# Performance work log

Measured on AMD Instinct MI355X. Metric: run time of the kernel, lower is better.

Reference implementation:

```python
import jax, jax.numpy as jnp
import numpy as np

K = 2  # num_experts_per_token


def setup_inputs() -> dict:
    key = jax.random.key(0)
    ks = jax.random.split(key, 5)
    B, T, D, E, H = 2, 2048, 768, 8, 1536
    x = jax.random.normal(ks[0], (B, T, D), dtype=jnp.float32)
    gate_w = jax.random.normal(ks[1], (E, D), dtype=jnp.float32) * (1.0 / np.sqrt(D))
    gate_bank = jax.random.normal(ks[2], (E, D, H), dtype=jnp.float32) * (1.0 / np.sqrt(D))
    up_bank = jax.random.normal(ks[3], (E, D, H), dtype=jnp.float32) * (1.0 / np.sqrt(D))
    down_bank = jax.random.normal(ks[4], (E, H, D), dtype=jnp.float32) * (1.0 / np.sqrt(H))
    return {"x": x, "gate_w": gate_w, "gate_bank": gate_bank,
            "up_bank": up_bank, "down_bank": down_bank}


def reference(x, gate_w, gate_bank, up_bank, down_bank):
    # x: [B,T,D]; gate_w: [E,D]; banks: [E,D,H]/[E,D,H]/[E,H,D]
    # Eval mode: no gate noise (module only adds noise when training).
    logits = jnp.einsum('btd,ed->bte', x, gate_w)                  # [B,T,E]
    probs = jax.nn.softmax(logits, axis=-1)
    selected_probs, selected_idx = jax.lax.top_k(probs, K)          # [B,T,K]
    selected_probs = selected_probs / (
        jnp.sum(selected_probs, axis=-1, keepdims=True) + 1e-8)

    a = jnp.einsum('btd,edh->bteh', x, gate_bank)                   # [B,T,E,H]
    u = jnp.einsum('btd,edh->bteh', x, up_bank)
    h = jax.nn.silu(a) * u
    y_all = jnp.einsum('bteh,ehd->bted', h, down_bank)              # [B,T,E,D]

    # Gather the top-k experts' outputs and combine with normalized weights.
    y_sel = jnp.take_along_axis(y_all, selected_idx[..., None], axis=2)  # [B,T,K,D]
    y = jnp.sum(y_sel * selected_probs[..., None], axis=2)          # [B,T,D]
    return y
```

## Files before the change

### kernel.cpp

```cpp
#include <hip/hip_runtime.h>
#include <hip/hip_bf16.h>

#define NTOK 4096
#define DDIM 768
#define EEXP 8
#define HDIM 1536
#define MBLK 128
#define MAXMB 72
#define CAP  (MAXMB * MBLK)
#define NENT (NTOK * 2)
#define RTHREADS 1024
#define EPT (NENT / RTHREADS)

typedef float f32x4 __attribute__((ext_vector_type(4)));
typedef __bf16 bf16x8 __attribute__((ext_vector_type(8)));
typedef __bf16 bf16x4 __attribute__((ext_vector_type(4)));

static const size_t XB_OFF   = 0;
static const size_t GT_OFF   = 6291456;
static const size_t UT_OFF   = GT_OFF + 18874368;
static const size_t YB_OFF   = GT_OFF;
static const size_t DT_OFF   = UT_OFF + 18874368;
static const size_t HB_OFF   = DT_OFF + 18874368;
static const size_t TKI_OFF  = HB_OFF + 28311552;
static const size_t TKW_OFF  = TKI_OFF + NENT*4;
static const size_t PT_OFF   = TKW_OFF + NENT*4;
static const size_t SL_OFF   = PT_OFF + CAP*4;
static const size_t CTRL_OFF = SL_OFF + NENT*4;
static const size_t WS_NEEDED = CTRL_OFF + 1024;

#define GLOAD16(g, l) __builtin_amdgcn_global_load_lds( \
    (const __attribute__((address_space(1))) void*)(g),  \
    (__attribute__((address_space(3))) void*)(l), 16, 0, 0)



__global__ __launch_bounds__(256) void convert_x_kernel(
    const float* __restrict__ x, __bf16* __restrict__ xb, int n4)
{
    int i = blockIdx.x * 256 + threadIdx.x;
    if (i < n4) {
        f32x4 v = reinterpret_cast<const f32x4*>(x)[i];
        bf16x4 o;
        o[0] = (__bf16)v[0]; o[1] = (__bf16)v[1];
        o[2] = (__bf16)v[2]; o[3] = (__bf16)v[3];
        reinterpret_cast<bf16x4*>(xb)[i] = o;
    }
}

__global__ __launch_bounds__(256) void transpose_bf16_kernel(
    const float* __restrict__ src, __bf16* __restrict__ dst, int R, int C)
{
    __shared__ float tile[32][33];
    const float* s = src + (size_t)blockIdx.z * R * C;
    __bf16* d = dst + (size_t)blockIdx.z * R * C;
    int tx = threadIdx.x & 31, ty = threadIdx.x >> 5;
    int r0 = blockIdx.y * 32, c0 = blockIdx.x * 32;
#pragma unroll
    for (int j = 0; j < 4; j++)
        tile[ty + j*8][tx] = s[(size_t)(r0 + ty + j*8) * C + c0 + tx];
    __syncthreads();
#pragma unroll
    for (int j = 0; j < 4; j++)
        d[(size_t)(c0 + ty + j*8) * R + r0 + tx] = (__bf16)tile[tx][ty + j*8];
}

__global__ __launch_bounds__(256) void gating_kernel(
    const float* __restrict__ x, const float* __restrict__ gw,
    int* __restrict__ topk_idx, float* __restrict__ topk_w)
{
    int lane = threadIdx.x & 63;
    int t = blockIdx.x * 4 + (threadIdx.x >> 6);
    const float* xr = x + (size_t)t * DDIM;
    float acc[EEXP];
#pragma unroll
    for (int e = 0; e < EEXP; e++) acc[e] = 0.0f;
    for (int i = 0; i < DDIM / 64; i++) {
        int d = lane + i * 64;
        float xv = xr[d];
#pragma unroll
        for (int e = 0; e < EEXP; e++) acc[e] += xv * gw[e * DDIM + d];
    }
#pragma unroll
    for (int e = 0; e < EEXP; e++) {
        for (int off = 32; off; off >>= 1) acc[e] += __shfl_xor(acc[e], off);
    }
    if (lane == 0) {
        float m = acc[0];
#pragma unroll
        for (int e = 1; e < EEXP; e++) m = fmaxf(m, acc[e]);
        float p[EEXP], sum = 0.0f;
#pragma unroll
        for (int e = 0; e < EEXP; e++) { p[e] = expf(acc[e] - m); sum += p[e]; }
        int i0 = 0; float b0 = acc[0];
#pragma unroll
        for (int e = 1; e < EEXP; e++) if (acc[e] > b0) { b0 = acc[e]; i0 = e; }
        int i1 = -1; float b1 = -3.4e38f;
#pragma unroll
        for (int e = 0; e < EEXP; e++) if (e != i0 && acc[e] > b1) { b1 = acc[e]; i1 = e; }
        float pr0 = p[i0] / sum, pr1 = p[i1] / sum;
        float den = pr0 + pr1 + 1e-8f;
        topk_idx[2*t]   = i0; topk_w[2*t]   = pr0 / den;
        topk_idx[2*t+1] = i1; topk_w[2*t+1] = pr1 / den;
    }
}

__global__ __launch_bounds__(RTHREADS) void route_kernel(
    const int* __restrict__ topk_idx, int* __restrict__ ctrl,
    int* __restrict__ pair_token, int* __restrict__ slot_of)
{
    __shared__ int wt[EEXP][16];
    __shared__ int wpre[EEXP][16];
    __shared__ int base[EEXP];

    int tid = threadIdx.x;
    int lane = tid & 63, wv = tid >> 6;

    for (int i = tid; i < CAP; i += RTHREADS) pair_token[i] = 0;

    int e_of[EPT];
    int c[EEXP];
#pragma unroll
    for (int e = 0; e < EEXP; e++) c[e] = 0;
#pragma unroll
    for (int j = 0; j < EPT; j++) {
        int e = topk_idx[tid * EPT + j];
        e_of[j] = e;
        c[e]++;
    }

    int pre[EEXP];
#pragma unroll
    for (int e = 0; e < EEXP; e++) {
        int v = c[e];
        for (int d = 1; d < 64; d <<= 1) {
            int u = __shfl_up(v, d);
            if (lane >= d) v += u;
        }
        pre[e] = v - c[e];
        if (lane == 63) wt[e][wv] = v;
    }
    __syncthreads();

    if (tid == 0) {
        int off = 0, gmb = 0;
        for (int e = 0; e < EEXP; e++) {
            int run = 0;
            for (int w = 0; w < 16; w++) { wpre[e][w] = run; run += wt[e][w]; }
            base[e] = off;
            int nmb = (run + MBLK - 1) >> 7;
            for (int i = 0; i < nmb; i++) ctrl[32 + gmb++] = e;
            off += nmb << 7;
        }
        ctrl[24] = gmb;
    }
    __syncthreads();

    int run[EEXP];
#pragma unroll
    for (int e = 0; e < EEXP; e++) run[e] = base[e] + wpre[e][wv] + pre[e];
#pragma unroll
    for (int j = 0; j < EPT; j++) {
        int ent = tid * EPT + j;
        int e = e_of[j];
        int slot = run[e]++;
        pair_token[slot] = ent >> 1;
        slot_of[ent] = slot;
    }
}

__global__ __launch_bounds__(512, 2) void gateup_kernel(
    const __bf16* __restrict__ xb, const __bf16* __restrict__ Gt,
    const __bf16* __restrict__ Ut, const int* __restrict__ ctrl,
    const int* __restrict__ pair_token, __bf16* __restrict__ hbuf)
{
    int bid = blockIdx.x;
    int swz = (bid & 7) * (MAXMB * 12 / 8) + (bid >> 3);
    int mb = swz / 12, y = swz - mb * 12;
    if (mb >= ctrl[24]) return;
    int e = ctrl[32 + mb];
    int hbase = y * 128;
    const __bf16* G = Gt + (size_t)e * HDIM * DDIM;
    const __bf16* U = Ut + (size_t)e * HDIM * DDIM;

    __shared__ __bf16 lds[2 * 3 * 8192];

    int tid = threadIdx.x;
    int lane = tid & 63, w = tid >> 6;
    int wr = w >> 2, wc = w & 3;

    int lr = tid >> 3;
    int lc = ((tid & 7) ^ (lr & 7)) << 3;
    int tok0 = pair_token[mb * MBLK + lr];
    int tok1 = pair_token[mb * MBLK + 64 + lr];
    const __bf16* gA0 = xb + (size_t)tok0 * DDIM + lc;
    const __bf16* gA1 = xb + (size_t)tok1 * DDIM + lc;
    const __bf16* gG0 = G + (size_t)(hbase + lr) * DDIM + lc;
    const __bf16* gU0 = U + (size_t)(hbase + lr) * DDIM + lc;
    const size_t bstep = (size_t)64 * DDIM;

    f32x4 accg[4][2], accu[4][2];
#pragma unroll
    for (int m = 0; m < 4; m++)
#pragma unroll
        for (int n = 0; n < 2; n++) { accg[m][n] = (f32x4)0.0f; accu[m][n] = (f32x4)0.0f; }

    {
        __bf16* d = &lds[0];
        GLOAD16(gA0, d + tid * 8);
        GLOAD16(gA1, d + 4096 + tid * 8);
        GLOAD16(gG0, d + 8192 + tid * 8);
        GLOAD16(gG0 + bstep, d + 12288 + tid * 8);
        GLOAD16(gU0, d + 16384 + tid * 8);
        GLOAD16(gU0 + bstep, d + 20480 + tid * 8);
    }
    __syncthreads();

    int cur = 0;
    for (int t = 0; t < DDIM / 64; ++t) {
        if (t < DDIM / 64 - 1) {
            int kk = (t + 1) * 64;
            __bf16* d = &lds[(cur ^ 1) * 24576];
            GLOAD16(gA0 + kk, d + tid * 8);
            GLOAD16(gA1 + kk, d + 4096 + tid * 8);
            GLOAD16(gG0 + kk, d + 8192 + tid * 8);
            GLOAD16(gG0 + kk + bstep, d + 12288 + tid * 8);
            GLOAD16(gU0 + kk, d + 16384 + tid * 8);
            GLOAD16(gU0 + kk + bstep, d + 20480 + tid * 8);
        }
        const __bf16* A  = &lds[cur * 24576];
        const __bf16* Bg = A + 8192;
        const __bf16* Bu = A + 16384;
#pragma unroll
        for (int ks = 0; ks < 2; ks++) {
            int kb = ks * 32 + (lane >> 4) * 8;
            bf16x8 af[4];
#pragma unroll
            for (int m = 0; m < 4; m++) {
                int row = wr * 64 + m * 16 + (lane & 15);
                af[m] = *reinterpret_cast<const bf16x8*>(
                    &A[row * 64 + (kb ^ ((row & 7) << 3))]);
            }
#pragma unroll
            for (int n = 0; n < 2; n++) {
                int col = wc * 32 + n * 16 + (lane & 15);
                int ba = col * 64 + (kb ^ ((col & 7) << 3));
                bf16x8 bg = *reinterpret_cast<const bf16x8*>(&Bg[ba]);
                bf16x8 bu = *reinterpret_cast<const bf16x8*>(&Bu[ba]);
#pragma unroll
                for (int m = 0; m < 4; m++) {
                    accg[m][n] = __builtin_amdgcn_mfma_f32_16x16x32_bf16(af[m], bg, accg[m][n], 0, 0, 0);
                    accu[m][n] = __builtin_amdgcn_mfma_f32_16x16x32_bf16(af[m], bu, accu[m][n], 0, 0, 0);
                }
            }
        }
        __syncthreads();
        cur ^= 1;
    }

    size_t slotbase = (size_t)mb * MBLK;
#pragma unroll
    for (int m = 0; m < 4; m++)
#pragma unroll
        for (int n = 0; n < 2; n++)
#pragma unroll
            for (int r = 0; r < 4; r++) {
                int row = wr * 64 + m * 16 + (lane >> 4) * 4 + r;
                int col = hbase + wc * 32 + n * 16 + (lane & 15);
                float a = accg[m][n][r], u = accu[m][n][r];
                float hv = (a / (1.0f + expf(-a))) * u;
                hbuf[(slotbase + row) * HDIM + col] = (__bf16)hv;
            }
}

__global__ __launch_bounds__(512, 4) void down_kernel(
    const __bf16* __restrict__ hbuf, const __bf16* __restrict__ Dt,
    const int* __restrict__ ctrl, float* __restrict__ ybuf)
{
    int bid = blockIdx.x;
    int swz = (bid & 7) * (MAXMB * 6 / 8) + (bid >> 3);
    int mb = swz / 6, y = swz - mb * 6;
    if (mb >= ctrl[24]) return;
    int e = ctrl[32 + mb];
    int dbase = y * 128;
    const __bf16* Dn = Dt + (size_t)e * DDIM * HDIM;

    __shared__ __bf16 lds[2 * 2 * 8192];

    int tid = threadIdx.x;
    int lane = tid & 63, w = tid >> 6;
    int wr = w >> 2, wc = w & 3;

    int lr = tid >> 3;
    int lc = ((tid & 7) ^ (lr & 7)) << 3;
    const __bf16* gA0 = hbuf + (size_t)(mb * MBLK + lr) * HDIM + lc;
    const __bf16* gB0 = Dn + (size_t)(dbase + lr) * HDIM + lc;
    const size_t astep = (size_t)64 * HDIM;

    f32x4 acc[4][2];
#pragma unroll
    for (int m = 0; m < 4; m++)
#pragma unroll
        for (int n = 0; n < 2; n++) acc[m][n] = (f32x4)0.0f;

    {
        __bf16* d = &lds[0];
        GLOAD16(gA0, d + tid * 8);
        GLOAD16(gA0 + astep, d + 4096 + tid * 8);
        GLOAD16(gB0, d + 8192 + tid * 8);
        GLOAD16(gB0 + astep, d + 12288 + tid * 8);
    }
    __syncthreads();

    int cur = 0;
    for (int t = 0; t < HDIM / 64; ++t) {
        if (t < HDIM / 64 - 1) {
            int kk = (t + 1) * 64;
            __bf16* d = &lds[(cur ^ 1) * 16384];
            GLOAD16(gA0 + kk, d + tid * 8);
            GLOAD16(gA0 + kk + astep, d + 4096 + tid * 8);
            GLOAD16(gB0 + kk, d + 8192 + tid * 8);
            GLOAD16(gB0 + kk + astep, d + 12288 + tid * 8);
        }
        const __bf16* A = &lds[cur * 16384];
        const __bf16* B = A + 8192;
#pragma unroll
        for (int ks = 0; ks < 2; ks++) {
            int kb = ks * 32 + (lane >> 4) * 8;
            bf16x8 af[4];
#pragma unroll
            for (int m = 0; m < 4; m++) {
                int row = wr * 64 + m * 16 + (lane & 15);
                af[m] = *reinterpret_cast<const bf16x8*>(
                    &A[row * 64 + (kb ^ ((row & 7) << 3))]);
            }
#pragma unroll
            for (int n = 0; n < 2; n++) {
                int col = wc * 32 + n * 16 + (lane & 15);
                bf16x8 bd = *reinterpret_cast<const bf16x8*>(
                    &B[col * 64 + (kb ^ ((col & 7) << 3))]);
#pragma unroll
                for (int m = 0; m < 4; m++)
                    acc[m][n] = __builtin_amdgcn_mfma_f32_16x16x32_bf16(af[m], bd, acc[m][n], 0, 0, 0);
            }
        }
        __syncthreads();
        cur ^= 1;
    }

#pragma unroll
    for (int m = 0; m < 4; m++)
#pragma unroll
        for (int n = 0; n < 2; n++)
#pragma unroll
            for (int r = 0; r < 4; r++) {
                int row = wr * 64 + m * 16 + (lane >> 4) * 4 + r;
                int col = dbase + wc * 32 + n * 16 + (lane & 15);
                ybuf[(size_t)(mb * MBLK + row) * DDIM + col] = acc[m][n][r];
            }
}

__global__ __launch_bounds__(192) void combine_kernel(
    const float* __restrict__ ybuf, const int* __restrict__ slot_of,
    const float* __restrict__ topk_w, float* __restrict__ out)
{
    int t = blockIdx.x;
    int q = threadIdx.x;
    int s0 = slot_of[2*t], s1 = slot_of[2*t+1];
    float w0 = topk_w[2*t], w1 = topk_w[2*t+1];
    f32x4 y0 = reinterpret_cast<const f32x4*>(ybuf + (size_t)s0 * DDIM)[q];
    f32x4 y1 = reinterpret_cast<const f32x4*>(ybuf + (size_t)s1 * DDIM)[q];
    f32x4 o;
#pragma unroll
    for (int r = 0; r < 4; r++) o[r] = w0 * y0[r] + w1 * y1[r];
    reinterpret_cast<f32x4*>(out + (size_t)t * DDIM)[q] = o;
}

extern "C" void kernel_launch(void* const* d_in, const int* in_sizes, int n_in,
                              void* d_out, int out_size, void* d_ws, size_t ws_size,
                              hipStream_t stream)
{
    if (ws_size < WS_NEEDED) return;

    const float* x      = (const float*)d_in[0];
    const float* gate_w = (const float*)d_in[1];
    const float* gbank  = (const float*)d_in[2];
    const float* ubank  = (const float*)d_in[3];
    const float* dbank  = (const float*)d_in[4];
    float* out = (float*)d_out;

    char* ws = (char*)d_ws;
    __bf16* xb   = (__bf16*)(ws + XB_OFF);
    __bf16* Gt   = (__bf16*)(ws + GT_OFF);
    __bf16* Ut   = (__bf16*)(ws + UT_OFF);
    float*  ybuf = (float*)(ws + YB_OFF);
    __bf16* Dt   = (__bf16*)(ws + DT_OFF);
    __bf16* hbuf = (__bf16*)(ws + HB_OFF);
    int*    tki  = (int*)(ws + TKI_OFF);
    float*  tkw  = (float*)(ws + TKW_OFF);
    int*    pt   = (int*)(ws + PT_OFF);
    int*    slot = (int*)(ws + SL_OFF);
    int*    ctrl = (int*)(ws + CTRL_OFF);

    convert_x_kernel<<<(NTOK * DDIM / 4 + 255) / 256, 256, 0, stream>>>(x, xb, NTOK * DDIM / 4);

    transpose_bf16_kernel<<<dim3(HDIM/32, DDIM/32, EEXP), 256, 0, stream>>>(gbank, Gt, DDIM, HDIM);
    transpose_bf16_kernel<<<dim3(HDIM/32, DDIM/32, EEXP), 256, 0, stream>>>(ubank, Ut, DDIM, HDIM);
    transpose_bf16_kernel<<<dim3(DDIM/32, HDIM/32, EEXP), 256, 0, stream>>>(dbank, Dt, HDIM, DDIM);

    gating_kernel<<<NTOK / 4, 256, 0, stream>>>(x, gate_w, tki, tkw);
    route_kernel<<<1, RTHREADS, 0, stream>>>(tki, ctrl, pt, slot);

    gateup_kernel<<<MAXMB * (HDIM / 128), 512, 0, stream>>>(xb, Gt, Ut, ctrl, pt, hbuf);
    down_kernel<<<MAXMB * (DDIM / 128), 512, 0, stream>>>(hbuf, Dt, ctrl, ybuf);
    combine_kernel<<<NTOK, 192, 0, stream>>>(ybuf, slot, tkw, out);
}
```

Before: 149.6 us.

## Triple-buffer gate/up GEMM with explicit vmcnt waits and vectorize weight transposes

The gate/up grouped GEMM moves from a double-buffered to a triple-buffered LDS pipeline that issues loads two stages ahead. It replaces __syncthreads with explicit vmcnt waits, scheduling barriers and raw s_barrier, and raises wave priority around the MFMA blocks; the down GEMM gets the same explicit-wait and priority treatment. The weight transposes switch to 64x64 tiles with float4 loads and bf16x4 stores to reduce per-element memory traffic overhead. The tripled LDS footprint in gateup (144KB at 512 threads) may not fit, or may cut occupancy against the launch bound of 2 blocks per CU.

New measurement: 152.0 us. About the same (+1.6%).

```diff
diff --git a/kernel.cpp b/kernel.cpp
--- a/kernel.cpp
+++ b/kernel.cpp
@@ -33,6 +33,10 @@
     (const __attribute__((address_space(1))) void*)(g),  \
     (__attribute__((address_space(3))) void*)(l), 16, 0, 0)
 
+#define VMWAIT(N) asm volatile("s_waitcnt vmcnt(" #N ")" ::: "memory")
+#define SFENCE()  __builtin_amdgcn_sched_barrier(0)
+#define BAR()     __builtin_amdgcn_s_barrier()
+
 
 
 __global__ __launch_bounds__(256) void convert_x_kernel(
@@ -48,21 +52,30 @@
     }
 }
 
-__global__ __launch_bounds__(256) void transpose_bf16_kernel(
+__global__ __launch_bounds__(256) void transpose64_kernel(
     const float* __restrict__ src, __bf16* __restrict__ dst, int R, int C)
 {
-    __shared__ float tile[32][33];
+    __shared__ float tile[64][65];
     const float* s = src + (size_t)blockIdx.z * R * C;
     __bf16* d = dst + (size_t)blockIdx.z * R * C;
-    int tx = threadIdx.x & 31, ty = threadIdx.x >> 5;
-    int r0 = blockIdx.y * 32, c0 = blockIdx.x * 32;
-#pragma unroll
-    for (int j = 0; j < 4; j++)
-        tile[ty + j*8][tx] = s[(size_t)(r0 + ty + j*8) * C + c0 + tx];
+    int tx = threadIdx.x & 15, ty = threadIdx.x >> 4;
+    int r0 = blockIdx.y * 64, c0 = blockIdx.x * 64;
+#pragma unroll
+    for (int j = 0; j < 4; j++) {
+        int r = ty + j * 16;
+        f32x4 v = *reinterpret_cast<const f32x4*>(&s[(size_t)(r0 + r) * C + c0 + tx * 4]);
+        tile[r][tx*4+0] = v[0]; tile[r][tx*4+1] = v[1];
+        tile[r][tx*4+2] = v[2]; tile[r][tx*4+3] = v[3];
+    }
     __syncthreads();
 #pragma unroll
-    for (int j = 0; j < 4; j++)
-        d[(size_t)(c0 + ty + j*8) * R + r0 + tx] = (__bf16)tile[tx][ty + j*8];
+    for (int j = 0; j < 4; j++) {
+        int c = ty + j * 16;
+        bf16x4 o;
+#pragma unroll
+        for (int i = 0; i < 4; i++) o[i] = (__bf16)tile[tx*4+i][c];
+        *reinterpret_cast<bf16x4*>(&d[(size_t)(c0 + c) * R + r0 + tx*4]) = o;
+    }
 }
 
 __global__ __launch_bounds__(256) void gating_kernel(
@@ -183,7 +196,7 @@
     const __bf16* G = Gt + (size_t)e * HDIM * DDIM;
     const __bf16* U = Ut + (size_t)e * HDIM * DDIM;
 
-    __shared__ __bf16 lds[2 * 3 * 8192];
+    __shared__ __bf16 lds[3 * 24576];
 
     int tid = threadIdx.x;
     int lane = tid & 63, w = tid >> 6;
@@ -205,30 +218,30 @@
 #pragma unroll
         for (int n = 0; n < 2; n++) { accg[m][n] = (f32x4)0.0f; accu[m][n] = (f32x4)0.0f; }
 
-    {
-        __bf16* d = &lds[0];
-        GLOAD16(gA0, d + tid * 8);
-        GLOAD16(gA1, d + 4096 + tid * 8);
-        GLOAD16(gG0, d + 8192 + tid * 8);
-        GLOAD16(gG0 + bstep, d + 12288 + tid * 8);
-        GLOAD16(gU0, d + 16384 + tid * 8);
-        GLOAD16(gU0 + bstep, d + 20480 + tid * 8);
-    }
-    __syncthreads();
-
-    int cur = 0;
-    for (int t = 0; t < DDIM / 64; ++t) {
-        if (t < DDIM / 64 - 1) {
-            int kk = (t + 1) * 64;
-            __bf16* d = &lds[(cur ^ 1) * 24576];
-            GLOAD16(gA0 + kk, d + tid * 8);
-            GLOAD16(gA1 + kk, d + 4096 + tid * 8);
-            GLOAD16(gG0 + kk, d + 8192 + tid * 8);
-            GLOAD16(gG0 + kk + bstep, d + 12288 + tid * 8);
-            GLOAD16(gU0 + kk, d + 16384 + tid * 8);
-            GLOAD16(gU0 + kk + bstep, d + 20480 + tid * 8);
-        }
-        const __bf16* A  = &lds[cur * 24576];
+    auto stage = [&](int buf, int kk) {
+        __bf16* d = &lds[buf * 24576];
+        GLOAD16(gA0 + kk, d + tid * 8);
+        GLOAD16(gA1 + kk, d + 4096 + tid * 8);
+        GLOAD16(gG0 + kk, d + 8192 + tid * 8);
+        GLOAD16(gG0 + kk + bstep, d + 12288 + tid * 8);
+        GLOAD16(gU0 + kk, d + 16384 + tid * 8);
+        GLOAD16(gU0 + kk + bstep, d + 20480 + tid * 8);
+    };
+
+    stage(0, 0);
+    stage(1, 64);
+    SFENCE();
+
+#pragma unroll
+    for (int t = 0; t < 12; ++t) {
+        if (t < 10) stage((t + 2) % 3, (t + 2) * 64);
+        SFENCE();
+        if (t < 10) { VMWAIT(12); } else if (t == 10) { VMWAIT(6); } else { VMWAIT(0); }
+        SFENCE();
+        BAR();
+        SFENCE();
+
+        const __bf16* A  = &lds[(t % 3) * 24576];
         const __bf16* Bg = A + 8192;
         const __bf16* Bu = A + 16384;
 #pragma unroll
@@ -241,6 +254,7 @@
                 af[m] = *reinterpret_cast<const bf16x8*>(
                     &A[row * 64 + (kb ^ ((row & 7) << 3))]);
             }
+            __builtin_amdgcn_s_setprio(1);
 #pragma unroll
             for (int n = 0; n < 2; n++) {
                 int col = wc * 32 + n * 16 + (lane & 15);
@@ -253,9 +267,11 @@
                     accu[m][n] = __builtin_amdgcn_mfma_f32_16x16x32_bf16(af[m], bu, accu[m][n], 0, 0, 0);
                 }
             }
+            __builtin_amdgcn_s_setprio(0);
         }
-        __syncthreads();
-        cur ^= 1;
+        SFENCE();
+        BAR();
+        SFENCE();
     }
 
     size_t slotbase = (size_t)mb * MBLK;
@@ -285,7 +301,7 @@
     int dbase = y * 128;
     const __bf16* Dn = Dt + (size_t)e * DDIM * HDIM;
 
-    __shared__ __bf16 lds[2 * 2 * 8192];
+    __shared__ __bf16 lds[2 * 16384];
 
     int tid = threadIdx.x;
     int lane = tid & 63, w = tid >> 6;
@@ -303,26 +319,27 @@
 #pragma unroll
         for (int n = 0; n < 2; n++) acc[m][n] = (f32x4)0.0f;
 
-    {
-        __bf16* d = &lds[0];
-        GLOAD16(gA0, d + tid * 8);
-        GLOAD16(gA0 + astep, d + 4096 + tid * 8);
-        GLOAD16(gB0, d + 8192 + tid * 8);
-        GLOAD16(gB0 + astep, d + 12288 + tid * 8);
-    }
-    __syncthreads();
-
-    int cur = 0;
-    for (int t = 0; t < HDIM / 64; ++t) {
-        if (t < HDIM / 64 - 1) {
-            int kk = (t + 1) * 64;
-            __bf16* d = &lds[(cur ^ 1) * 16384];
-            GLOAD16(gA0 + kk, d + tid * 8);
-            GLOAD16(gA0 + kk + astep, d + 4096 + tid * 8);
-            GLOAD16(gB0 + kk, d + 8192 + tid * 8);
-            GLOAD16(gB0 + kk + astep, d + 12288 + tid * 8);
-        }
-        const __bf16* A = &lds[cur * 16384];
+    auto stage = [&](int buf, int kk) {
+        __bf16* d = &lds[buf * 16384];
+        GLOAD16(gA0 + kk, d + tid * 8);
+        GLOAD16(gA0 + kk + astep, d + 4096 + tid * 8);
+        GLOAD16(gB0 + kk, d + 8192 + tid * 8);
+        GLOAD16(gB0 + kk + astep, d + 12288 + tid * 8);
+    };
+
+    stage(0, 0);
+    SFENCE();
+
+#pragma unroll
+    for (int t = 0; t < 24; ++t) {
+        if (t < 23) stage((t + 1) & 1, (t + 1) * 64);
+        SFENCE();
+        if (t < 23) { VMWAIT(4); } else { VMWAIT(0); }
+        SFENCE();
+        BAR();
+        SFENCE();
+
+        const __bf16* A = &lds[(t & 1) * 16384];
         const __bf16* B = A + 8192;
 #pragma unroll
         for (int ks = 0; ks < 2; ks++) {
@@ -334,6 +351,7 @@
                 af[m] = *reinterpret_cast<const bf16x8*>(
                     &A[row * 64 + (kb ^ ((row & 7) << 3))]);
             }
+            __builtin_amdgcn_s_setprio(1);
 #pragma unroll
             for (int n = 0; n < 2; n++) {
                 int col = wc * 32 + n * 16 + (lane & 15);
@@ -343,9 +361,11 @@
                 for (int m = 0; m < 4; m++)
                     acc[m][n] = __builtin_amdgcn_mfma_f32_16x16x32_bf16(af[m], bd, acc[m][n], 0, 0, 0);
             }
+            __builtin_amdgcn_s_setprio(0);
         }
-        __syncthreads();
-        cur ^= 1;
+        SFENCE();
+        BAR();
+        SFENCE();
     }
 
 #pragma unroll
@@ -404,9 +424,9 @@
 
     convert_x_kernel<<<(NTOK * DDIM / 4 + 255) / 256, 256, 0, stream>>>(x, xb, NTOK * DDIM / 4);
 
-    transpose_bf16_kernel<<<dim3(HDIM/32, DDIM/32, EEXP), 256, 0, stream>>>(gbank, Gt, DDIM, HDIM);
-    transpose_bf16_kernel<<<dim3(HDIM/32, DDIM/32, EEXP), 256, 0, stream>>>(ubank, Ut, DDIM, HDIM);
-    transpose_bf16_kernel<<<dim3(DDIM/32, HDIM/32, EEXP), 256, 0, stream>>>(dbank, Dt, HDIM, DDIM);
+    transpose64_kernel<<<dim3(HDIM/64, DDIM/64, EEXP), 256, 0, stream>>>(gbank, Gt, DDIM, HDIM);
+    transpose64_kernel<<<dim3(HDIM/64, DDIM/64, EEXP), 256, 0, stream>>>(ubank, Ut, DDIM, HDIM);
+    transpose64_kernel<<<dim3(DDIM/64, HDIM/64, EEXP), 256, 0, stream>>>(dbank, Dt, HDIM, DDIM);
 
     gating_kernel<<<NTOK / 4, 256, 0, stream>>>(x, gate_w, tki, tkw);
     route_kernel<<<1, RTHREADS, 0, stream>>>(tki, ctrl, pt, slot);
```
